# Kernel optimization log

Hardware: AMD Instinct MI355X
Metric: run time of the kernel (lower is better)

Reference implementation:

```python
import jax, jax.numpy as jnp
import numpy as np

K = 4
TEMPERATURE = 34.0
IN_CH = 256
OUT_CH = 256
KSIZE = 3
PAD = 1
HIDDEN = int(2 * IN_CH * 0.25) + 1  # pool_mode='mix' doubles channels -> 129


def setup_inputs() -> dict:
    key = jax.random.key(0)
    ks = jax.random.split(key, 6)
    x = jax.random.normal(ks[0], (32, IN_CH, 56, 56), dtype=jnp.float32)
    # dynamic kernel bank [K, O, C, k, k]
    weight = jax.random.normal(ks[1], (K, OUT_CH, IN_CH, KSIZE, KSIZE), dtype=jnp.float32) * 0.05
    bias_k = jnp.zeros((K, OUT_CH), dtype=jnp.float32)
    # attention MLP (1x1 convs on pooled [B, 2C, 1, 1] == linear layers)
    w1 = jax.random.normal(ks[2], (HIDDEN, 2 * IN_CH), dtype=jnp.float32) * 0.06  # fc1, no bias
    w2 = jax.random.normal(ks[3], (K, HIDDEN), dtype=jnp.float32) * 0.12
    b2 = jnp.zeros((K,), dtype=jnp.float32)
    return {"x": x, "weight": weight, "bias_k": bias_k, "w1": w1, "w2": w2, "b2": b2}


def _attention(x, w1, w2, b2):
    # mix pooling: concat(avg, max) over spatial dims -> [B, 2C]
    avg = jnp.mean(x, axis=(2, 3))
    mx = jnp.max(x, axis=(2, 3))
    p = jnp.concatenate([avg, mx], axis=1)
    h = jax.nn.relu(jnp.einsum('bc,hc->bh', p, w1))
    logits = jnp.einsum('bh,kh->bk', h, w2) + b2
    return jax.nn.softmax(logits / TEMPERATURE, axis=1)  # [B, K]


def reference(x, weight, bias_k, w1, w2, b2):
    B, C, H, W = x.shape
    attn = _attention(x, w1, w2, b2)  # [B, K]
    # per-sample aggregated kernels [B, O, C, k, k]
    agg_w = jnp.einsum('bk,kocuv->bocuv', attn, weight)
    agg_b = attn @ bias_k  # [B, O]
    # grouped-conv trick: treat batch as groups
    xg = x.reshape(1, B * C, H, W)
    wg = agg_w.reshape(B * OUT_CH, C, KSIZE, KSIZE)
    out = jax.lax.conv_general_dilated(
        xg, wg,
        window_strides=(1, 1),
        padding=[(PAD, PAD), (PAD, PAD)],
        dimension_numbers=('NCHW', 'OIHW', 'NCHW'),
        feature_group_count=B,
    )  # [1, B*O, H, W]
    out = out.reshape(B, OUT_CH, H, W) + agg_b[:, :, None, None]
    return out
```

## Files before the change

kernel.cpp:

```cpp
#include <hip/hip_runtime.h>
#include <math.h>

#define BB 32
#define CC 256
#define OO 256
#define HW 56
#define SP (HW*HW)
#define KK 4
#define HID 129
#define TEMP 34.0f
#define PROW 58
#define PLANE (PROW*PROW*32)
#define PLANEB (PROW*PROW*64)
#define NSLOT 348
#define QSLOT 350
#define QSTRIDE (QSLOT*16)
#define NPIECE (4*QSLOT)
#define XA_B 8192
#define XB_B 24576

typedef unsigned short u16;
typedef unsigned int uint32;
typedef __attribute__((ext_vector_type(8))) short bf16x8;
typedef __attribute__((ext_vector_type(4))) float f32x4;

#define WAITVM(n) asm volatile("s_waitcnt vmcnt(" #n ")" ::: "memory")
#define WAITLGKM() asm volatile("s_waitcnt lgkmcnt(0)" ::: "memory")

__device__ __forceinline__ u16 f2bf(float f) {
    union { float f; uint32 u; } v; v.f = f;
    uint32 r = v.u + 0x7FFF + ((v.u >> 16) & 1);
    return (u16)(r >> 16);
}

__device__ __forceinline__ void gload16(const void* g, void* l) {
    __builtin_amdgcn_global_load_lds(
        (const __attribute__((address_space(1))) unsigned int*)g,
        (__attribute__((address_space(3))) unsigned int*)l, 16, 0, 0);
}

__global__ __launch_bounds__(256) void trans_pool(const float* __restrict__ x,
                                                  u16* __restrict__ xt,
                                                  float* __restrict__ pooled) {
    const int cb = blockIdx.x, b = blockIdx.y;
    const int tid = threadIdx.x;
    const int lane = tid & 63, wave = tid >> 6;
    const float* xp = x + ((size_t)b * CC + cb * 32) * SP;
    u16* xtb = xt + (size_t)(b * 8 + cb) * PLANE;

    if (tid < 228) {
        int slot;
        if (tid < 58)       slot = tid;
        else if (tid < 116) slot = 57 * 58 + (tid - 58);
        else if (tid < 172) slot = (tid - 116 + 1) * 58;
        else                slot = (tid - 172 + 1) * 58 + 57;
        bf16x8 z = {};
        #pragma unroll
        for (int j = 0; j < 4; ++j)
            *(bf16x8*)&xtb[(size_t)slot * 32 + j * 8] = z;
    }

    float psum[32], pmax[32];
    #pragma unroll
    for (int c = 0; c < 32; ++c) { psum[c] = 0.f; pmax[c] = -INFINITY; }

    for (int p0 = 0; p0 < SP; p0 += 256) {
        const int p = p0 + tid;
        const bool v = p < SP;
        const int pc = v ? p : (SP - 1);
        u16 ob[32];
        #pragma unroll
        for (int c = 0; c < 32; ++c) {
            const float vv = xp[(size_t)c * SP + pc];
            if (v) { psum[c] += vv; pmax[c] = fmaxf(pmax[c], vv); }
            ob[c] = f2bf(vv);
        }
        if (v) {
            const int slot = (p / 56 + 1) * 58 + (p % 56 + 1);
            #pragma unroll
            for (int j = 0; j < 4; ++j)
                *(bf16x8*)&xtb[(size_t)slot * 32 + j * 8] = *(bf16x8*)&ob[j * 8];
        }
    }
    #pragma unroll
    for (int c = 0; c < 32; ++c) {
        #pragma unroll
        for (int off = 32; off >= 1; off >>= 1) {
            psum[c] += __shfl_xor(psum[c], off, 64);
            pmax[c] = fmaxf(pmax[c], __shfl_xor(pmax[c], off, 64));
        }
    }
    __shared__ float ssum[4][32];
    __shared__ float smax[4][32];
    if (lane == 0) {
        #pragma unroll
        for (int c = 0; c < 32; ++c) { ssum[wave][c] = psum[c]; smax[wave][c] = pmax[c]; }
    }
    __syncthreads();
    if (tid < 32) {
        const float s = ssum[0][tid] + ssum[1][tid] + ssum[2][tid] + ssum[3][tid];
        const float m = fmaxf(fmaxf(smax[0][tid], smax[1][tid]),
                              fmaxf(smax[2][tid], smax[3][tid]));
        pooled[b * (2 * CC) + cb * 32 + tid]      = s / (float)SP;
        pooled[b * (2 * CC) + CC + cb * 32 + tid] = m;
    }
}

__global__ __launch_bounds__(256) void attn_kernel(const float* __restrict__ pooled,
                                                   const float* __restrict__ w1,
                                                   const float* __restrict__ w2,
                                                   const float* __restrict__ b2,
                                                   const float* __restrict__ bias_k,
                                                   float* __restrict__ attn,
                                                   float* __restrict__ agg_b) {
    const int b = blockIdx.x;
    const int tid = threadIdx.x;
    __shared__ float p[2 * CC];
    __shared__ float h[HID];
    __shared__ float a[KK];
    for (int i = tid; i < 2 * CC; i += 256) p[i] = pooled[b * 2 * CC + i];
    __syncthreads();
    if (tid < HID) {
        float s = 0.f;
        const float* w1r = w1 + (size_t)tid * (2 * CC);
        for (int c = 0; c < 2 * CC; ++c) s = fmaf(p[c], w1r[c], s);
        h[tid] = fmaxf(s, 0.f);
    }
    __syncthreads();
    if (tid == 0) {
        float lg[KK];
        float m = -INFINITY;
        for (int k = 0; k < KK; ++k) {
            float s = b2[k];
            for (int i = 0; i < HID; ++i) s = fmaf(h[i], w2[k * HID + i], s);
            lg[k] = s / TEMP;
            m = fmaxf(m, lg[k]);
        }
        float den = 0.f;
        for (int k = 0; k < KK; ++k) { lg[k] = expf(lg[k] - m); den += lg[k]; }
        for (int k = 0; k < KK; ++k) { a[k] = lg[k] / den; attn[b * KK + k] = a[k]; }
    }
    __syncthreads();
    if (tid < OO) {
        float s = 0.f;
        #pragma unroll
        for (int k = 0; k < KK; ++k) s = fmaf(a[k], bias_k[k * OO + tid], s);
        agg_b[b * OO + tid] = s;
    }
}

__global__ __launch_bounds__(256) void agg_kernel(const float* __restrict__ weight,
                                                  const float* __restrict__ attn,
                                                  u16* __restrict__ wT2) {
    const int o = blockIdx.x;
    const int c = threadIdx.x;
    __shared__ float at[BB * KK];
    if (threadIdx.x < BB * KK) at[threadIdx.x] = attn[threadIdx.x];
    __syncthreads();
    float w[KK][9];
    #pragma unroll
    for (int k = 0; k < KK; ++k)
        #pragma unroll
        for (int uv = 0; uv < 9; ++uv)
            w[k][uv] = weight[(size_t)((k * OO + o) * CC + c) * 9 + uv];
    const int cb = c >> 5, kg = (c >> 3) & 3, cl = c & 7;
    const int oy = o >> 7, ol = o & 127;
    const size_t sub = (size_t)kg * 1024 + ol * 8 + cl;
    for (int b = 0; b < BB; ++b) {
        const float a0 = at[b*KK+0], a1 = at[b*KK+1], a2 = at[b*KK+2], a3 = at[b*KK+3];
        #pragma unroll
        for (int uv = 0; uv < 9; ++uv) {
            float s = a0 * w[0][uv] + a1 * w[1][uv] + a2 * w[2][uv] + a3 * w[3][uv];
            const size_t region = (((size_t)b * 9 + uv) * 8 + cb) * 2 + oy;
            wT2[region * 4096 + sub] = f2bf(s);
        }
    }
}

__global__ __launch_bounds__(512, 4) void conv_mfma(const u16* __restrict__ xt,
                                                    const u16* __restrict__ wT2,
                                                    const float* __restrict__ agg_b,
                                                    float* __restrict__ out) {
    const int id   = blockIdx.x;
    const int g    = id >> 3;
    const int b    = (id & 7) + 8 * (g / 28);
    const int tile = g % 28;
    const int px   = tile % 14, oy = tile / 14;
    const int tid  = threadIdx.x;
    const int lane = tid & 63, wave = tid >> 6;
    const int wm = wave & 3, wn = wave >> 2;
    const int l15 = lane & 15, kg = lane >> 4;
    const int p0 = px * 224;

    __shared__ char XA[3][XA_B];
    __shared__ char XB[2][XB_B];

    uint32 soff[3];
    #pragma unroll
    for (int k = 0; k < 3; ++k) {
        int i = k * 512 + tid;
        if (i >= NPIECE) i = NPIECE - 1;
        const int q = i / QSLOT, slot = i % QSLOT;
        soff[k] = (uint32)((px * 232 + slot) * 64 + q * 16);
    }

    int bboff[7];
    #pragma unroll
    for (int nf = 0; nf < 7; ++nf) {
        const int n = wn * 112 + nf * 16 + l15;
        const int S = (n / 56 + 1) * 58 + (n % 56 + 1);
        bboff[nf] = kg * QSTRIDE + S * 16;
    }

    const int aoff0 = kg * 2048 + (wm * 32 + l15) * 16;
    const int aoff1 = aoff0 + 16 * 16;

    const char* xgb = (const char*)xt + (size_t)(b * 8) * PLANEB;
    const char* wAb = (const char*)wT2 + (size_t)b * 9 * 8 * 2 * 8192
                     + (size_t)oy * 8192;
    const size_t tb = (size_t)tid * 16;

    f32x4 acc[2][7];
    #pragma unroll
    for (int mf = 0; mf < 2; ++mf)
        #pragma unroll
        for (int nf = 0; nf < 7; ++nf)
            acc[mf][nf] = (f32x4)0.f;

    #pragma unroll
    for (int k = 0; k < 3; ++k)
        gload16(xgb + soff[k], &XB[0][k * 8192 + wave * 1024]);
    gload16(wAb + (size_t)(0 * 8 + 0) * 2 * 8192 + tb, &XA[0][wave * 1024]);
    gload16(wAb + (size_t)(1 * 8 + 0) * 2 * 8192 + tb, &XA[1][wave * 1024]);

    for (int cb = 0; cb < 8; ++cb) {
        const char* RB = XB[cb & 1];
        char* WB = XB[(cb & 1) ^ 1];
        const char* xg_next = xgb + (size_t)((cb + 1) & 7) * PLANEB;

        #pragma unroll
        for (int uv = 0; uv < 9; ++uv) {
            if (uv == 2 || uv == 3) WAITVM(3);
            else if (uv == 1 || uv == 4) WAITVM(2);
            else WAITVM(1);
            __builtin_amdgcn_s_barrier();

            const char* RA = XA[uv % 3];
            bf16x8 av0 = *(const bf16x8*)(RA + aoff0);
            bf16x8 av1 = *(const bf16x8*)(RA + aoff1);
            const int dby = ((uv / 3 - 1) * 58 + (uv % 3 - 1)) * 16;
            bf16x8 bv[7];
            #pragma unroll
            for (int nf = 0; nf < 7; ++nf)
                bv[nf] = *(const bf16x8*)(RB + bboff[nf] + dby);

            {
                const int uv_s = (uv + 2 < 9) ? uv + 2 : uv - 7;
                const int cb_s = (uv + 2 < 9) ? cb : ((cb + 1) & 7);
                gload16(wAb + (size_t)(uv_s * 8 + cb_s) * 2 * 8192 + tb,
                        &XA[(uv + 2) % 3][wave * 1024]);
            }
            if (uv < 3)
                gload16(xg_next + soff[uv], &WB[uv * 8192 + wave * 1024]);

            WAITLGKM();
            __builtin_amdgcn_sched_barrier(0);
            __builtin_amdgcn_s_setprio(1);
            #pragma unroll
            for (int nf = 0; nf < 7; ++nf) {
                acc[0][nf] = __builtin_amdgcn_mfma_f32_16x16x32_bf16(av0, bv[nf], acc[0][nf], 0, 0, 0);
                acc[1][nf] = __builtin_amdgcn_mfma_f32_16x16x32_bf16(av1, bv[nf], acc[1][nf], 0, 0, 0);
            }
            __builtin_amdgcn_s_setprio(0);
        }
    }

    const int obase = oy * 128 + wm * 32;
    float* outb = out + (size_t)b * OO * SP;
    #pragma unroll
    for (int mf = 0; mf < 2; ++mf) {
        #pragma unroll
        for (int r = 0; r < 4; ++r) {
            const int o = obase + mf * 16 + kg * 4 + r;
            const float bias = agg_b[b * OO + o];
            #pragma unroll
            for (int nf = 0; nf < 7; ++nf) {
                const int p = p0 + wn * 112 + nf * 16 + l15;
                outb[(size_t)o * SP + p] = acc[mf][nf][r] + bias;
            }
        }
    }
}

extern "C" void kernel_launch(void* const* d_in, const int* in_sizes, int n_in,
                              void* d_out, int out_size, void* d_ws, size_t ws_size,
                              hipStream_t stream) {
    const float* x      = (const float*)d_in[0];
    const float* weight = (const float*)d_in[1];
    const float* bias_k = (const float*)d_in[2];
    const float* w1     = (const float*)d_in[3];
    const float* w2     = (const float*)d_in[4];
    const float* b2     = (const float*)d_in[5];
    float* out = (float*)d_out;

    u16* x_t = (u16*)d_ws;
    u16* wT2 = x_t + (size_t)BB * 8 * PLANE;
    float* ws_f   = (float*)(wT2 + (size_t)BB * 9 * OO * CC);
    float* pooled = ws_f;
    float* attn   = ws_f + BB * 2 * CC;
    float* agg_b  = attn + BB * KK;

    trans_pool<<<dim3(8, BB), 256, 0, stream>>>(x, x_t, pooled);
    attn_kernel<<<BB, 256, 0, stream>>>(pooled, w1, w2, b2, bias_k, attn, agg_b);
    agg_kernel<<<OO, 256, 0, stream>>>(weight, attn, wT2);
    conv_mfma<<<896, 512, 0, stream>>>(x_t, wT2, agg_b, out);
}
```

Baseline: 207.0 us.

## Restructure aggregation kernel for 16-byte vectorized bf16 weight stores

Remaps the per-sample kernel aggregation so each thread owns 8 consecutive input channels for one output channel. Each thread now writes one 16-byte bf16x8 vector per (batch, tap) instead of scattered 2-byte stores. The grid changes from 256 blocks to 64 blocks of 512 threads, split over channel-block/row-half and batch groups. The aim is less store-transaction overhead on the large wT2 buffer, at the cost of strided per-tap weight loads that are re-read across batch groups, and fewer blocks in flight.

```diff
diff --git a/kernel.cpp b/kernel.cpp
--- a/kernel.cpp
+++ b/kernel.cpp
@@ -149,30 +149,37 @@
     }
 }
 
-__global__ __launch_bounds__(256) void agg_kernel(const float* __restrict__ weight,
+__global__ __launch_bounds__(512) void agg_kernel(const float* __restrict__ weight,
                                                   const float* __restrict__ attn,
                                                   u16* __restrict__ wT2) {
-    const int o = blockIdx.x;
-    const int c = threadIdx.x;
+    const int oycb = blockIdx.x;
+    const int oy = oycb & 1, cb = oycb >> 1;
+    const int bg = blockIdx.y;
+    const int tid = threadIdx.x;
+    const int kg = tid >> 7, ol = tid & 127;
+    const int o = oy * 128 + ol;
+    const int cbase = cb * 32 + kg * 8;
     __shared__ float at[BB * KK];
-    if (threadIdx.x < BB * KK) at[threadIdx.x] = attn[threadIdx.x];
-    __syncthreads();
-    float w[KK][9];
-    #pragma unroll
-    for (int k = 0; k < KK; ++k)
-        #pragma unroll
-        for (int uv = 0; uv < 9; ++uv)
-            w[k][uv] = weight[(size_t)((k * OO + o) * CC + c) * 9 + uv];
-    const int cb = c >> 5, kg = (c >> 3) & 3, cl = c & 7;
-    const int oy = o >> 7, ol = o & 127;
-    const size_t sub = (size_t)kg * 1024 + ol * 8 + cl;
-    for (int b = 0; b < BB; ++b) {
-        const float a0 = at[b*KK+0], a1 = at[b*KK+1], a2 = at[b*KK+2], a3 = at[b*KK+3];
-        #pragma unroll
-        for (int uv = 0; uv < 9; ++uv) {
-            float s = a0 * w[0][uv] + a1 * w[1][uv] + a2 * w[2][uv] + a3 * w[3][uv];
+    if (tid < BB * KK) at[tid] = attn[tid];
+    __syncthreads();
+    const size_t sub = (size_t)kg * 1024 + ol * 8;
+    for (int uv = 0; uv < 9; ++uv) {
+        float w[KK][8];
+        #pragma unroll
+        for (int k = 0; k < KK; ++k)
+            #pragma unroll
+            for (int cl = 0; cl < 8; ++cl)
+                w[k][cl] = weight[(size_t)((k * OO + o) * CC + cbase + cl) * 9 + uv];
+        #pragma unroll
+        for (int b8 = 0; b8 < 8; ++b8) {
+            const int b = bg * 8 + b8;
+            const float a0 = at[b*KK+0], a1 = at[b*KK+1], a2 = at[b*KK+2], a3 = at[b*KK+3];
+            u16 ob[8];
+            #pragma unroll
+            for (int cl = 0; cl < 8; ++cl)
+                ob[cl] = f2bf(a0 * w[0][cl] + a1 * w[1][cl] + a2 * w[2][cl] + a3 * w[3][cl]);
             const size_t region = (((size_t)b * 9 + uv) * 8 + cb) * 2 + oy;
-            wT2[region * 4096 + sub] = f2bf(s);
+            *(bf16x8*)&wT2[region * 4096 + sub] = *(bf16x8*)ob;
         }
     }
 }
@@ -312,6 +319,6 @@
 
     trans_pool<<<dim3(8, BB), 256, 0, stream>>>(x, x_t, pooled);
     attn_kernel<<<BB, 256, 0, stream>>>(pooled, w1, w2, b2, bias_k, attn, agg_b);
-    agg_kernel<<<OO, 256, 0, stream>>>(weight, attn, wT2);
+    agg_kernel<<<dim3(16, 4), 512, 0, stream>>>(weight, attn, wT2);
     conv_mfma<<<896, 512, 0, stream>>>(x_t, wT2, agg_b, out);
 }
```

Result: slower. 255.0 us (+23.2%).
